# Optimization experiments

Hardware: AMD Instinct MI355X
Metric: run time of the kernel (lower is better)

Reference implementation:

```python
import jax, jax.numpy as jnp
import numpy as np

N, DX, DZ, DY, H = 8192, 64, 128, 16, 512


def setup_inputs() -> dict:
    key = jax.random.key(0)
    ks = jax.random.split(key, 8)
    s1 = 1.0 / np.sqrt(DX)
    s2 = 1.0 / np.sqrt(H)
    return {
        "z_pred": jax.random.normal(ks[0], (N, DZ), dtype=jnp.float32),
        "x_label": jax.random.normal(ks[1], (N, DX), dtype=jnp.float32),
        "y_label": jax.random.normal(ks[2], (N, DY), dtype=jnp.float32),
        "W1": jax.random.normal(ks[3], (DX, H), dtype=jnp.float32) * s1,
        "b1": jnp.zeros((H,), dtype=jnp.float32),
        "W2": jax.random.normal(ks[4], (H, DZ), dtype=jnp.float32) * s2,
        "b2": jnp.zeros((DZ,), dtype=jnp.float32),
        "A": jax.random.normal(ks[5], (DZ, DZ), dtype=jnp.float32) * (1.0 / np.sqrt(DZ)),
        "B": jax.random.normal(ks[6], (DZ, DY), dtype=jnp.float32) * (1.0 / np.sqrt(DY)),
    }


def reference(z_pred, x_label, y_label, W1, b1, W2, b2, A, B):
    # forward_mapper T: x (dx,) -> (dz,), 2-layer tanh MLP
    def T(x):
        return jnp.tanh(x @ W1 + b1) @ W2 + b2

    # diff_eq: per-sample nonlinear dynamics x_dot = tanh(x)
    x_dot = jnp.tanh(x_label)  # (N, dx)

    # per-sample Jacobian dT/dx: (N, dz, dx). Equivalent to the torch code's
    # full N x N batched Jacobian followed by the diagonal slice, but without
    # the O(N^2) waste.
    jac = jax.vmap(jax.jacrev(T))(x_label)  # (N, dz, dx)

    dtdx_mul_f = jnp.einsum("nzd,nd->nz", jac, x_dot)  # (N, dz)
    m_mul_t = z_pred @ A.T                              # (N, dz)
    k_mul_h = y_label @ B.T                             # (N, dz)

    pde = dtdx_mul_f - m_mul_t - k_mul_h                # (N, dz)
    loss_batch = jnp.linalg.norm(pde, axis=1)           # (N,)
    return jnp.mean(loss_batch)
```

## Files before the change

### kernel.cpp

```cpp
#include <hip/hip_runtime.h>
#include <math.h>

#define Nn   8192
#define DXc  64
#define DZc  128
#define DYc  16
#define Hc   512
#define NKC  21

typedef short bf16x8 __attribute__((ext_vector_type(8)));
typedef float f32x4  __attribute__((ext_vector_type(4)));

__device__ __forceinline__ float fast_tanh(float x) {
    float e = __expf(2.0f * x);
    return 1.0f - 2.0f / (e + 1.0f);
}
__device__ __forceinline__ short f2bf(float f) {
    unsigned u = __float_as_uint(f);
    return (short)((u + 0x7FFFu + ((u >> 16) & 1u)) >> 16);
}
__device__ __forceinline__ bf16x8 pack8(float4 a, float4 b) {
    bf16x8 r;
    r[0]=f2bf(a.x); r[1]=f2bf(a.y); r[2]=f2bf(a.z); r[3]=f2bf(a.w);
    r[4]=f2bf(b.x); r[5]=f2bf(b.y); r[6]=f2bf(b.z); r[7]=f2bf(b.w);
    return r;
}

__global__ void prep_kernel(const float* __restrict__ W1,
                            const float* __restrict__ W2,
                            const float* __restrict__ A,
                            const float* __restrict__ Bm,
                            short* __restrict__ Wb,
                            short* __restrict__ Wf,
                            float* __restrict__ out) {
    __shared__ float tile[64 * 129];
    const int blk = blockIdx.x, t = threadIdx.x;

    if (blk < 8) {
        const int jb = blk * 64;
#pragma unroll
        for (int p = 0; p < 16; p++) {
            int lin = p * 256 + t;
            int k = lin >> 6, jj = lin & 63;
            tile[jj * 65 + k] = W1[(size_t)k * Hc + jb + jj];
        }
        __syncthreads();
#pragma unroll
        for (int p = 0; p < 2; p++) {
            int cid = p * 256 + t;
            int lane = cid & 63, q = lane >> 4, n16 = lane & 15;
            int kc2 = (cid >> 6) & 1, jt4 = cid >> 7;
            int jl = jt4 * 16 + n16, k0 = kc2 * 32 + q * 8;
            bf16x8 v;
#pragma unroll
            for (int i = 0; i < 8; i++) v[i] = f2bf(tile[jl * 65 + k0 + i]);
            int block = ((blk * 4 + jt4) * 2 + kc2);
            *(bf16x8*)(Wb + (size_t)(block * 64 + lane) * 8) = v;
        }
    } else if (blk < 16) {
        const int kb = (blk - 8) * 64;
#pragma unroll
        for (int p = 0; p < 32; p++) {
            int lin = p * 256 + t;
            int kk = lin >> 7, z = lin & 127;
            tile[kk * 129 + z] = W2[(size_t)(kb + kk) * DZc + z];
        }
        __syncthreads();
#pragma unroll
        for (int p = 0; p < 4; p++) {
            int cid = p * 256 + t;
            int lane = cid & 63, q = lane >> 4, n16 = lane & 15;
            int rest = cid >> 6;
            int kc2 = rest & 1, zt = rest >> 1;
            int z = zt * 16 + n16, k0l = kc2 * 32 + q * 8;
            bf16x8 v;
#pragma unroll
            for (int i = 0; i < 8; i++) v[i] = f2bf(tile[(k0l + i) * 129 + z]);
            int kc = (kb >> 5) + kc2;
            *(bf16x8*)(Wf + (size_t)((zt * NKC + kc) * 64 + lane) * 8) = v;
        }
    } else if (blk < 24) {
        int cid = (blk - 16) * 256 + t;
        int lane = cid & 63, q = lane >> 4, n16 = lane & 15;
        int rest = cid >> 6;
        int kcl = rest & 3, zt = rest >> 2;
        int z = zt * 16 + n16, c0 = kcl * 32 + q * 8;
        float4 a0 = *(const float4*)(A + (size_t)z * DZc + c0);
        float4 a1 = *(const float4*)(A + (size_t)z * DZc + c0 + 4);
        bf16x8 v;
        v[0]=f2bf(-a0.x); v[1]=f2bf(-a0.y); v[2]=f2bf(-a0.z); v[3]=f2bf(-a0.w);
        v[4]=f2bf(-a1.x); v[5]=f2bf(-a1.y); v[6]=f2bf(-a1.z); v[7]=f2bf(-a1.w);
        *(bf16x8*)(Wf + (size_t)((zt * NKC + 16 + kcl) * 64 + lane) * 8) = v;
    } else {
        if (t == 0) out[0] = 0.f;
#pragma unroll
        for (int p = 0; p < 2; p++) {
            int cid = p * 256 + t;
            int lane = cid & 63, q = lane >> 4, n16 = lane & 15;
            int zt = cid >> 6;
            int z = zt * 16 + n16;
            bf16x8 v = (bf16x8){0,0,0,0,0,0,0,0};
            if (q < 2) {
                float4 b0 = *(const float4*)(Bm + (size_t)z * DYc + q * 8);
                float4 b1 = *(const float4*)(Bm + (size_t)z * DYc + q * 8 + 4);
                v[0]=f2bf(-b0.x); v[1]=f2bf(-b0.y); v[2]=f2bf(-b0.z); v[3]=f2bf(-b0.w);
                v[4]=f2bf(-b1.x); v[5]=f2bf(-b1.y); v[6]=f2bf(-b1.z); v[7]=f2bf(-b1.w);
            }
            *(bf16x8*)(Wf + (size_t)((zt * NKC + 20) * 64 + lane) * 8) = v;
        }
    }
}

#define MFMA16(a, b, c) __builtin_amdgcn_mfma_f32_16x16x32_bf16((a), (b), (c), 0, 0, 0)

__global__ __launch_bounds__(256, 4)
void pde_main(const float* __restrict__ z_pred,
              const float* __restrict__ x_label,
              const float* __restrict__ y_label,
              const float* __restrict__ b1,
              const short* __restrict__ Wb,
              const short* __restrict__ Wf,
              float* __restrict__ out) {
    __shared__ __align__(16) short sS[16 * 512];
    __shared__ float red[4][16];

    const int tid  = threadIdx.x;
    const int w    = tid >> 6;
    const int lane = tid & 63;
    const int n16  = lane & 15;
    const int q    = lane >> 4;
    const int n0   = blockIdx.x * 16;

    const float* xp = x_label + (size_t)(n0 + n16) * DXc + q * 8;
    float4 x0 = *(const float4*)xp,        x1 = *(const float4*)(xp + 4);
    float4 x2 = *(const float4*)(xp + 32), x3 = *(const float4*)(xp + 36);
    bf16x8 ax0 = pack8(x0, x1), ax1 = pack8(x2, x3);
    bf16x8 at0, at1;
    {
        float v[16] = {x0.x,x0.y,x0.z,x0.w, x1.x,x1.y,x1.z,x1.w,
                       x2.x,x2.y,x2.z,x2.w, x3.x,x3.y,x3.z,x3.w};
#pragma unroll
        for (int i = 0; i < 8; i++) { at0[i] = f2bf(fast_tanh(v[i])); at1[i] = f2bf(fast_tanh(v[8 + i])); }
    }

#pragma unroll
    for (int t = 0; t < 8; t++) {
        const int jt = 8 * w + t;
        const short* bp = Wb + (size_t)(jt * 2 * 64 + lane) * 8;
        bf16x8 bw0 = *(const bf16x8*)bp;
        bf16x8 bw1 = *(const bf16x8*)(bp + 512);
        f32x4 h = (f32x4){0.f,0.f,0.f,0.f};
        f32x4 u = (f32x4){0.f,0.f,0.f,0.f};
        h = MFMA16(ax0, bw0, h);  h = MFMA16(ax1, bw1, h);
        u = MFMA16(at0, bw0, u);  u = MFMA16(at1, bw1, u);
        const float bj = b1[jt * 16 + n16];
        const int j = jt * 16 + n16;
        const int sbase = (j >> 5) * 512 + ((j >> 3) & 3) * 128 + (j & 7);
#pragma unroll
        for (int reg = 0; reg < 4; reg++) {
            float tv = fast_tanh(h[reg] + bj);
            float s  = (1.f - tv * tv) * u[reg];
            sS[sbase + (q * 4 + reg) * 8] = f2bf(s);
        }
    }

    const short* wf0 = Wf + (size_t)((2 * w)     * NKC * 64 + lane) * 8;
    const short* wf1 = Wf + (size_t)((2 * w + 1) * NKC * 64 + lane) * 8;
    f32x4 acc0 = (f32x4){0.f,0.f,0.f,0.f};
    f32x4 acc1 = (f32x4){0.f,0.f,0.f,0.f};
    {
        const float* zp = z_pred + (size_t)(n0 + n16) * DZc + q * 8;
#pragma unroll
        for (int kcl = 0; kcl < 4; kcl++) {
            float4 a0 = *(const float4*)(zp + kcl * 32);
            float4 a1 = *(const float4*)(zp + kcl * 32 + 4);
            bf16x8 az = pack8(a0, a1);
            acc0 = MFMA16(az, *(const bf16x8*)(wf0 + (16 + kcl) * 512), acc0);
            acc1 = MFMA16(az, *(const bf16x8*)(wf1 + (16 + kcl) * 512), acc1);
        }
        bf16x8 ay = (bf16x8){0,0,0,0,0,0,0,0};
        if (q < 2) {
            const float* yp = y_label + (size_t)(n0 + n16) * DYc + q * 8;
            ay = pack8(*(const float4*)yp, *(const float4*)(yp + 4));
        }
        acc0 = MFMA16(ay, *(const bf16x8*)(wf0 + 20 * 512), acc0);
        acc1 = MFMA16(ay, *(const bf16x8*)(wf1 + 20 * 512), acc1);
    }

    bf16x8 pf0[4], pf1[4];
#pragma unroll
    for (int c = 0; c < 4; c++) {
        pf0[c] = *(const bf16x8*)(wf0 + c * 512);
        pf1[c] = *(const bf16x8*)(wf1 + c * 512);
    }

    __syncthreads();

#pragma unroll
    for (int kc = 0; kc < 16; kc++) {
        bf16x8 sa = *(const bf16x8*)(sS + kc * 512 + lane * 8);
        bf16x8 b0 = (kc < 4) ? pf0[kc & 3] : *(const bf16x8*)(wf0 + kc * 512);
        bf16x8 b1f = (kc < 4) ? pf1[kc & 3] : *(const bf16x8*)(wf1 + kc * 512);
        acc0 = MFMA16(sa, b0, acc0);
        acc1 = MFMA16(sa, b1f, acc1);
    }

#pragma unroll
    for (int reg = 0; reg < 4; reg++) {
        float sq = fmaf(acc0[reg], acc0[reg], acc1[reg] * acc1[reg]);
        sq += __shfl_xor(sq, 1);
        sq += __shfl_xor(sq, 2);
        sq += __shfl_xor(sq, 4);
        sq += __shfl_xor(sq, 8);
        if (n16 == 0) red[w][q * 4 + reg] = sq;
    }
    __syncthreads();

    if (tid < 16) {
        float tot = red[0][tid] + red[1][tid] + red[2][tid] + red[3][tid];
        float nrm = sqrtf(tot);
        nrm += __shfl_xor(nrm, 1);
        nrm += __shfl_xor(nrm, 2);
        nrm += __shfl_xor(nrm, 4);
        nrm += __shfl_xor(nrm, 8);
        if (tid == 0) atomicAdd(out, nrm * (1.0f / (float)Nn));
    }
}

extern "C" void kernel_launch(void* const* d_in, const int* in_sizes, int n_in,
                              void* d_out, int out_size, void* d_ws, size_t ws_size,
                              hipStream_t stream) {
    const float* z_pred  = (const float*)d_in[0];
    const float* x_label = (const float*)d_in[1];
    const float* y_label = (const float*)d_in[2];
    const float* W1      = (const float*)d_in[3];
    const float* b1      = (const float*)d_in[4];
    const float* W2      = (const float*)d_in[5];
    const float* A       = (const float*)d_in[7];
    const float* Bm      = (const float*)d_in[8];

    short* Wb = (short*)d_ws;
    short* Wf = Wb + 512 * DXc;

    prep_kernel<<<25, 256, 0, stream>>>(W1, W2, A, Bm, Wb, Wf, (float*)d_out);
    pde_main<<<Nn / 16, 256, 0, stream>>>(z_pred, x_label, y_label, b1, Wb, Wf, (float*)d_out);
}
```

Before: 93.77 us.

## Flatten weight-prep kernel to one chunk per thread and drop prefetch

The weight-packing prep kernel drops its shared-memory transpose and has each thread gather and pack one 8-element bf16 chunk straight from global memory. The grid grows from 25 to 58 blocks to cover all chunks. The main kernel also stops prefetching the first four W2 fragments into registers before the barrier, which lowers register pressure but leaves those loads exposed. The uncoalesced strided gathers in prep may cost more, though that kernel is small.

```diff
diff --git a/kernel.cpp b/kernel.cpp
--- a/kernel.cpp
+++ b/kernel.cpp
@@ -26,88 +26,50 @@
     return r;
 }
 
-__global__ void prep_kernel(const float* __restrict__ W1,
-                            const float* __restrict__ W2,
-                            const float* __restrict__ A,
-                            const float* __restrict__ Bm,
-                            short* __restrict__ Wb,
-                            short* __restrict__ Wf,
-                            float* __restrict__ out) {
-    __shared__ float tile[64 * 129];
-    const int blk = blockIdx.x, t = threadIdx.x;
-
-    if (blk < 8) {
-        const int jb = blk * 64;
-#pragma unroll
-        for (int p = 0; p < 16; p++) {
-            int lin = p * 256 + t;
-            int k = lin >> 6, jj = lin & 63;
-            tile[jj * 65 + k] = W1[(size_t)k * Hc + jb + jj];
-        }
-        __syncthreads();
-#pragma unroll
-        for (int p = 0; p < 2; p++) {
-            int cid = p * 256 + t;
-            int lane = cid & 63, q = lane >> 4, n16 = lane & 15;
-            int kc2 = (cid >> 6) & 1, jt4 = cid >> 7;
-            int jl = jt4 * 16 + n16, k0 = kc2 * 32 + q * 8;
-            bf16x8 v;
-#pragma unroll
-            for (int i = 0; i < 8; i++) v[i] = f2bf(tile[jl * 65 + k0 + i]);
-            int block = ((blk * 4 + jt4) * 2 + kc2);
-            *(bf16x8*)(Wb + (size_t)(block * 64 + lane) * 8) = v;
-        }
-    } else if (blk < 16) {
-        const int kb = (blk - 8) * 64;
-#pragma unroll
-        for (int p = 0; p < 32; p++) {
-            int lin = p * 256 + t;
-            int kk = lin >> 7, z = lin & 127;
-            tile[kk * 129 + z] = W2[(size_t)(kb + kk) * DZc + z];
-        }
-        __syncthreads();
-#pragma unroll
-        for (int p = 0; p < 4; p++) {
-            int cid = p * 256 + t;
-            int lane = cid & 63, q = lane >> 4, n16 = lane & 15;
-            int rest = cid >> 6;
-            int kc2 = rest & 1, zt = rest >> 1;
-            int z = zt * 16 + n16, k0l = kc2 * 32 + q * 8;
-            bf16x8 v;
-#pragma unroll
-            for (int i = 0; i < 8; i++) v[i] = f2bf(tile[(k0l + i) * 129 + z]);
-            int kc = (kb >> 5) + kc2;
-            *(bf16x8*)(Wf + (size_t)((zt * NKC + kc) * 64 + lane) * 8) = v;
-        }
-    } else if (blk < 24) {
-        int cid = (blk - 16) * 256 + t;
-        int lane = cid & 63, q = lane >> 4, n16 = lane & 15;
-        int rest = cid >> 6;
-        int kcl = rest & 3, zt = rest >> 2;
-        int z = zt * 16 + n16, c0 = kcl * 32 + q * 8;
-        float4 a0 = *(const float4*)(A + (size_t)z * DZc + c0);
-        float4 a1 = *(const float4*)(A + (size_t)z * DZc + c0 + 4);
+__global__ __launch_bounds__(256)
+void prep_kernel(const float* __restrict__ W1,
+                 const float* __restrict__ W2,
+                 const float* __restrict__ A,
+                 const float* __restrict__ Bm,
+                 short* __restrict__ Wb,
+                 short* __restrict__ Wf,
+                 float* __restrict__ out) {
+    int c = blockIdx.x * 256 + threadIdx.x;
+    if (c == 0) out[0] = 0.f;
+
+    if (c < 4096) {
+        int lane = c & 63, block = c >> 6;
+        int n16 = lane & 15, q = lane >> 4;
+        int j = (block >> 1) * 16 + n16;
+        int k0 = (block & 1) * 32 + q * 8;
         bf16x8 v;
-        v[0]=f2bf(-a0.x); v[1]=f2bf(-a0.y); v[2]=f2bf(-a0.z); v[3]=f2bf(-a0.w);
-        v[4]=f2bf(-a1.x); v[5]=f2bf(-a1.y); v[6]=f2bf(-a1.z); v[7]=f2bf(-a1.w);
-        *(bf16x8*)(Wf + (size_t)((zt * NKC + 16 + kcl) * 64 + lane) * 8) = v;
+#pragma unroll
+        for (int i = 0; i < 8; i++) v[i] = f2bf(W1[(size_t)(k0 + i) * Hc + j]);
+        *(bf16x8*)(Wb + (size_t)c * 8) = v;
     } else {
-        if (t == 0) out[0] = 0.f;
-#pragma unroll
-        for (int p = 0; p < 2; p++) {
-            int cid = p * 256 + t;
-            int lane = cid & 63, q = lane >> 4, n16 = lane & 15;
-            int zt = cid >> 6;
-            int z = zt * 16 + n16;
-            bf16x8 v = (bf16x8){0,0,0,0,0,0,0,0};
-            if (q < 2) {
-                float4 b0 = *(const float4*)(Bm + (size_t)z * DYc + q * 8);
-                float4 b1 = *(const float4*)(Bm + (size_t)z * DYc + q * 8 + 4);
-                v[0]=f2bf(-b0.x); v[1]=f2bf(-b0.y); v[2]=f2bf(-b0.z); v[3]=f2bf(-b0.w);
-                v[4]=f2bf(-b1.x); v[5]=f2bf(-b1.y); v[6]=f2bf(-b1.z); v[7]=f2bf(-b1.w);
-            }
-            *(bf16x8*)(Wf + (size_t)((zt * NKC + 20) * 64 + lane) * 8) = v;
-        }
+        int c2 = c - 4096;
+        int lane = c2 & 63, block = c2 >> 6;
+        int zt = block / 21, kc = block % 21;
+        int n16 = lane & 15, q = lane >> 4;
+        int z = zt * 16 + n16;
+        bf16x8 v = (bf16x8){0,0,0,0,0,0,0,0};
+        if (kc < 16) {
+            int k0 = kc * 32 + q * 8;
+#pragma unroll
+            for (int i = 0; i < 8; i++) v[i] = f2bf(W2[(size_t)(k0 + i) * DZc + z]);
+        } else if (kc < 20) {
+            int c0 = (kc - 16) * 32 + q * 8;
+            float4 a0 = *(const float4*)(A + (size_t)z * DZc + c0);
+            float4 a1 = *(const float4*)(A + (size_t)z * DZc + c0 + 4);
+            v[0]=f2bf(-a0.x); v[1]=f2bf(-a0.y); v[2]=f2bf(-a0.z); v[3]=f2bf(-a0.w);
+            v[4]=f2bf(-a1.x); v[5]=f2bf(-a1.y); v[6]=f2bf(-a1.z); v[7]=f2bf(-a1.w);
+        } else if (q < 2) {
+            float4 b0 = *(const float4*)(Bm + (size_t)z * DYc + q * 8);
+            float4 b1 = *(const float4*)(Bm + (size_t)z * DYc + q * 8 + 4);
+            v[0]=f2bf(-b0.x); v[1]=f2bf(-b0.y); v[2]=f2bf(-b0.z); v[3]=f2bf(-b0.w);
+            v[4]=f2bf(-b1.x); v[5]=f2bf(-b1.y); v[6]=f2bf(-b1.z); v[7]=f2bf(-b1.w);
+        }
+        *(bf16x8*)(Wf + (size_t)c2 * 8) = v;
     }
 }
 
@@ -187,22 +149,13 @@
         acc1 = MFMA16(ay, *(const bf16x8*)(wf1 + 20 * 512), acc1);
     }
 
-    bf16x8 pf0[4], pf1[4];
-#pragma unroll
-    for (int c = 0; c < 4; c++) {
-        pf0[c] = *(const bf16x8*)(wf0 + c * 512);
-        pf1[c] = *(const bf16x8*)(wf1 + c * 512);
-    }
-
     __syncthreads();
 
 #pragma unroll
     for (int kc = 0; kc < 16; kc++) {
         bf16x8 sa = *(const bf16x8*)(sS + kc * 512 + lane * 8);
-        bf16x8 b0 = (kc < 4) ? pf0[kc & 3] : *(const bf16x8*)(wf0 + kc * 512);
-        bf16x8 b1f = (kc < 4) ? pf1[kc & 3] : *(const bf16x8*)(wf1 + kc * 512);
-        acc0 = MFMA16(sa, b0, acc0);
-        acc1 = MFMA16(sa, b1f, acc1);
+        acc0 = MFMA16(sa, *(const bf16x8*)(wf0 + kc * 512), acc0);
+        acc1 = MFMA16(sa, *(const bf16x8*)(wf1 + kc * 512), acc1);
     }
 
 #pragma unroll
@@ -242,6 +195,6 @@
     short* Wb = (short*)d_ws;
     short* Wf = Wb + 512 * DXc;
 
-    prep_kernel<<<25, 256, 0, stream>>>(W1, W2, A, Bm, Wb, Wf, (float*)d_out);
+    prep_kernel<<<58, 256, 0, stream>>>(W1, W2, A, Bm, Wb, Wf, (float*)d_out);
     pde_main<<<Nn / 16, 256, 0, stream>>>(z_pred, x_label, y_label, b1, Wb, Wf, (float*)d_out);
 }
```

After: 86.75 us. -7.5%, faster.
